# Kernel tuning notes

Measured on AMD Instinct MI355X. Metric: run time of the kernel, lower is better.

The kernel has to match this reference:

```python
import jax, jax.numpy as jnp
import numpy as np

NUM_EMBEDDINGS = 1024
EMBEDDING_DIM = 256
COMMITMENT_COST = 0.25


def setup_inputs() -> dict:
    key = jax.random.key(0)
    k1, k2 = jax.random.split(key)
    x = jax.random.normal(k1, (16, 4096, EMBEDDING_DIM), dtype=jnp.float32)
    # torch init: uniform(-1/K, 1/K); keep same scale
    embedding_weight = jax.random.uniform(
        k2, (NUM_EMBEDDINGS, EMBEDDING_DIM), dtype=jnp.float32,
        minval=-1.0 / NUM_EMBEDDINGS, maxval=1.0 / NUM_EMBEDDINGS)
    return {"x": x, "embedding_weight": embedding_weight}


def reference(x, embedding_weight):
    original_shape = x.shape
    x_flat = x.reshape(-1, EMBEDDING_DIM)                     # [N, D]
    d2 = (jnp.sum(x_flat ** 2, axis=1, keepdims=True)
          + jnp.sum(embedding_weight ** 2, axis=1)
          - 2.0 * x_flat @ embedding_weight.T)                # [N, K]
    d2 = jnp.maximum(d2, 0.0)
    encoding_indices = jnp.argmin(d2, axis=1)                 # [N]
    quantized_flat = embedding_weight[encoding_indices]        # [N, D]
    quantized = quantized_flat.reshape(original_shape)

    q_sg = jax.lax.stop_gradient(quantized)
    codebook_loss = jnp.mean((q_sg - x) ** 2)
    commitment_loss = jnp.mean((x - q_sg) ** 2)
    vq_total_loss = codebook_loss + COMMITMENT_COST * commitment_loss

    # straight-through estimator
    quantized_st = x + jax.lax.stop_gradient(quantized - x)

    # perplexity via index counts (avoids materializing one-hot [N, K])
    n = x_flat.shape[0]
    counts = jnp.zeros((NUM_EMBEDDINGS,), jnp.float32).at[encoding_indices].add(1.0)
    avg_probs = counts / n
    perplexity = jnp.exp(-jnp.sum(avg_probs * jnp.log(avg_probs + 1e-10)))

    return quantized_st, vq_total_loss, perplexity, encoding_indices
```

## Files before the change

### kernel.cpp

```cpp
#include <hip/hip_runtime.h>
#include <math.h>

#define N_ROWS   65536
#define DIM      256
#define KCODES   1024
#define Q_SIZE   (N_ROWS * DIM)
#define OUT_LOSS Q_SIZE
#define OUT_PERP (Q_SIZE + 1)
#define OUT_IDX  (Q_SIZE + 2)

#define TAUP 200.0f

#define WS_LOSS   0
#define WS_RCNT   8
#define WS_E2     16
#define WS_E2P    4112
#define WS_COUNTS 8208
#define WS_IDX    12304
#define WS_RLIST  274448
#define WS_ET     536592
#define WS_P      1585168

typedef _Float16 half8 __attribute__((ext_vector_type(8)));
typedef _Float16 half4 __attribute__((ext_vector_type(4)));
typedef float    f32x4 __attribute__((ext_vector_type(4)));

#define ROWB 528
#define RPB  64

#define LDS_X  0
#define LDS_E2 33792
#define LDS_B  37888

__global__ void k_prep(const float* __restrict__ E, float* __restrict__ e2,
                       float* __restrict__ e2p, float* __restrict__ Et,
                       _Float16* __restrict__ P,
                       int* __restrict__ counts, double* __restrict__ loss,
                       int* __restrict__ rcnt) {
    int b = blockIdx.x, t = threadIdx.x;
    __shared__ double red[256];
    float v = E[b * DIM + t];
    red[t] = (double)v * (double)v;

    {
        int o   = b * 256 + t;
        int j    = o & 7;
        int lane = (o >> 3) & 63;
        int nt   = (o >> 9) & 3;
        int kk   = (o >> 11) & 7;
        int cbq  = o >> 14;
        int q = cbq >> 2, cb = cbq & 3;
        int code = q * 256 + cb * 64 + nt * 16 + (lane & 15);
        int d    = (lane >> 4) * 8 + kk * 32 + j;
        P[o] = (_Float16)(E[code * DIM + d] * 1024.0f);
    }

    __syncthreads();
    for (int s = 128; s > 0; s >>= 1) {
        if (t < s) red[t] += red[t + s];
        __syncthreads();
    }
    if (t == 0) { e2[b] = (float)red[0]; e2p[b] = (float)(red[0] * 1048576.0); }

    int o = b * 256 + t;
    int d = o >> 10, k = o & 1023;
    Et[o] = E[k * DIM + d];

    if (b < 4) counts[b * 256 + t] = 0;
    if (b == 0 && t == 0) { *loss = 0.0; *rcnt = 0; }
}

__launch_bounds__(256)
__global__ void k_main(const float* __restrict__ X, const _Float16* __restrict__ P,
                       const float* __restrict__ e2p,
                       int* __restrict__ idx_ws, int* __restrict__ rlist,
                       int* __restrict__ rcnt) {
    __shared__ __align__(16) char sAll[70656];
    const int tid  = threadIdx.x;
    const int wid  = tid >> 6;
    const int lane = tid & 63;
    const int c16  = lane & 15;
    const int kg   = lane >> 4;
    const int rb   = blockIdx.x * RPB;

    char* sA = sAll + LDS_X;

    {
        const float4* Xg = (const float4*)(X + (size_t)rb * DIM);
        #pragma unroll
        for (int it = 0; it < 16; ++it) {
            int f = it * 256 + tid;
            int row = f >> 6, d4 = f & 63;
            float4 v = Xg[(size_t)row * 64 + d4];
            half4 hh = {(_Float16)v.x, (_Float16)v.y, (_Float16)v.z, (_Float16)v.w};
            *(half4*)(sA + row * ROWB + d4 * 8) = hh;
        }
        ((float4*)(sAll + LDS_E2))[tid] = ((const float4*)e2p)[tid];
    }

    const char* gB = (const char*)P + (size_t)wid * 131072 + (size_t)lane * 16;
    char*       lB = sAll + LDS_B + wid * 8192;
#define GLL(ss, nt)                                                                          \
    __builtin_amdgcn_global_load_lds(                                                        \
        (const __attribute__((address_space(1))) unsigned int*)(gB + (size_t)(((ss) * 4 + (nt)) * 1024)), \
        (__attribute__((address_space(3))) unsigned int*)(lB + (((ss) & 1) * 4096 + (nt) * 1024)),        \
        16, 0, 0)
    GLL(0, 0); GLL(0, 1); GLL(0, 2); GLL(0, 3);
    GLL(1, 0); GLL(1, 1); GLL(1, 2); GLL(1, 3);

    __syncthreads();

    int Abase[4];
    #pragma unroll
    for (int mt = 0; mt < 4; ++mt) Abase[mt] = (mt * 16 + c16) * ROWB + kg * 16;

    float tb1[16], tb2[16];
    int   ti1[16];
    #pragma unroll
    for (int i = 0; i < 16; ++i) { tb1[i] = 3.4e38f; tb2[i] = 3.4e38f; ti1[i] = 0; }

    const int cw = wid * 256;
    const float* sE2 = (const float*)(sAll + LDS_E2);

    f32x4 acc[4][4];

    #pragma unroll
    for (int s = 0; s < 32; ++s) {
        const int cb = s >> 3, kk = s & 7;
        if (kk == 0) {
            #pragma unroll
            for (int mt = 0; mt < 4; ++mt)
                #pragma unroll
                for (int nt = 0; nt < 4; ++nt) acc[mt][nt] = 0.0f;
        }
        if (s == 31) { asm volatile("s_waitcnt vmcnt(0)" ::: "memory"); }
        else         { asm volatile("s_waitcnt vmcnt(4)" ::: "memory"); }
        __builtin_amdgcn_sched_barrier(0);

        const char* bb = lB + (s & 1) * 4096 + (size_t)lane * 16;
        half8 b0 = *(const half8*)(bb);
        half8 b1 = *(const half8*)(bb + 1024);
        half8 b2 = *(const half8*)(bb + 2048);
        half8 b3 = *(const half8*)(bb + 3072);
        half8 ah[4];
        #pragma unroll
        for (int mt = 0; mt < 4; ++mt)
            ah[mt] = *(const half8*)(sA + Abase[mt] + kk * 64);

        asm volatile("s_waitcnt lgkmcnt(0)" ::: "memory");
        __builtin_amdgcn_sched_barrier(0);
        if (s < 30) { GLL(s + 2, 0); GLL(s + 2, 1); GLL(s + 2, 2); GLL(s + 2, 3); }
        __builtin_amdgcn_sched_barrier(0);

        #pragma unroll
        for (int mt = 0; mt < 4; ++mt) {
            acc[mt][0] = __builtin_amdgcn_mfma_f32_16x16x32_f16(ah[mt], b0, acc[mt][0], 0, 0, 0);
            acc[mt][1] = __builtin_amdgcn_mfma_f32_16x16x32_f16(ah[mt], b1, acc[mt][1], 0, 0, 0);
            acc[mt][2] = __builtin_amdgcn_mfma_f32_16x16x32_f16(ah[mt], b2, acc[mt][2], 0, 0, 0);
            acc[mt][3] = __builtin_amdgcn_mfma_f32_16x16x32_f16(ah[mt], b3, acc[mt][3], 0, 0, 0);
        }

        if (kk == 7) {
            const int cbase = cw + cb * 64;
            const int c0 = cbase + c16;
            float e2v[4];
            #pragma unroll
            for (int nt = 0; nt < 4; ++nt) e2v[nt] = sE2[c0 + nt * 16];
            #pragma unroll
            for (int mt = 0; mt < 4; ++mt)
                #pragma unroll
                for (int nt = 0; nt < 4; ++nt) {
                    int code = cbase + nt * 16 + c16;
                    #pragma unroll
                    for (int r = 0; r < 4; ++r) {
                        float sc = fmaf(-2048.0f, acc[mt][nt][r], e2v[nt]);
                        int ix = mt * 4 + r;
                        float hi = fmaxf(tb1[ix], sc);
                        tb2[ix] = fminf(tb2[ix], hi);
                        bool lt = sc < tb1[ix];
                        tb1[ix] = lt ? sc : tb1[ix];
                        ti1[ix] = lt ? code : ti1[ix];
                    }
                }
        }
    }
#undef GLL

    #pragma unroll
    for (int ix = 0; ix < 16; ++ix) {
        float v1 = tb1[ix], v2 = tb2[ix];
        int   j1 = ti1[ix];
        #pragma unroll
        for (int m = 1; m < 16; m <<= 1) {
            float ov1 = __shfl_xor(v1, m, 64);
            int   oj1 = __shfl_xor(j1, m, 64);
            float ov2 = __shfl_xor(v2, m, 64);
            bool take = (ov1 < v1) || (ov1 == v1 && oj1 < j1);
            float losr = take ? v1 : ov1;
            v1 = take ? ov1 : v1;
            j1 = take ? oj1 : j1;
            v2 = fminf(fminf(v2, ov2), losr);
        }
        tb1[ix] = v1; tb2[ix] = v2; ti1[ix] = j1;
    }

    __syncthreads();
    float* mB1 = (float*)sA;
    float* mB2 = (float*)(sA + 1024);
    int*   mI1 = (int*)(sA + 2048);
    #pragma unroll
    for (int ix = 0; ix < 16; ++ix) {
        if (c16 == ix) {
            int row = (ix >> 2) * 16 + kg * 4 + (ix & 3);
            mB1[row * 4 + wid] = tb1[ix];
            mB2[row * 4 + wid] = tb2[ix];
            mI1[row * 4 + wid] = ti1[ix];
        }
    }
    __syncthreads();
    if (tid < RPB) {
        float m1 = 3.4e38f, m2 = 3.4e38f;
        int mi = 0;
        #pragma unroll
        for (int w = 0; w < 4; ++w) {
            float v = mB1[tid * 4 + w];
            int  id = mI1[tid * 4 + w];
            float u = mB2[tid * 4 + w];
            bool take = (v < m1) || (v == m1 && id < mi);
            float losr = take ? m1 : v;
            m1 = take ? v : m1;
            mi = take ? id : mi;
            m2 = fminf(fminf(m2, u), losr);
        }
        int g = rb + tid;
        idx_ws[g] = mi;
        if (m2 - m1 < TAUP) {
            int slot = atomicAdd(rcnt, 1);
            rlist[slot] = g;
        }
    }
}

__launch_bounds__(256, 1)
__global__ void k_refine(const float* __restrict__ X, const float* __restrict__ Et,
                         const float* __restrict__ e2,
                         const int* __restrict__ rlist, const int* __restrict__ rcnt,
                         int* __restrict__ idx_ws) {
    __shared__ float xs[4][256];
    __shared__ float sbv[4][256];
    __shared__ int   sbi[4][256];
    __shared__ float x2s[4];
    __shared__ int   rows[4];
    const int cnt = *rcnt;
    const int t = threadIdx.x;
    for (int base = blockIdx.x * 4; base < cnt; base += gridDim.x * 4) {
        __syncthreads();
        if (t < 4) {
            int e = base + t;
            rows[t] = rlist[e < cnt ? e : (cnt - 1)];
        }
        __syncthreads();
        ((float4*)xs[t >> 6])[t & 63] =
            ((const float4*)(X + (size_t)rows[t >> 6] * DIM))[t & 63];
        __syncthreads();
        if (t < 4) {
            double s = 0.0;
            for (int d = 0; d < DIM; ++d) { double xv = (double)xs[t][d]; s += xv * xv; }
            x2s[t] = (float)s;
        }
        __syncthreads();

        double a0[4], a1[4], a2[4], a3[4];
        #pragma unroll
        for (int r = 0; r < 4; ++r) { a0[r] = 0.0; a1[r] = 0.0; a2[r] = 0.0; a3[r] = 0.0; }
        for (int d = 0; d < DIM; ++d) {
            double e0 = (double)Et[d * KCODES + t];
            double e1 = (double)Et[d * KCODES + 256 + t];
            double e2d = (double)Et[d * KCODES + 512 + t];
            double e3 = (double)Et[d * KCODES + 768 + t];
            #pragma unroll
            for (int r = 0; r < 4; ++r) {
                double xv = (double)xs[r][d];
                a0[r] += xv * e0;
                a1[r] += xv * e1;
                a2[r] += xv * e2d;
                a3[r] += xv * e3;
            }
        }

        const float eA = e2[t], eB = e2[256 + t], eC = e2[512 + t], eD = e2[768 + t];
        #pragma unroll
        for (int r = 0; r < 4; ++r) {
            float best = 3.4e38f; int bk = 0;
            float x2 = x2s[r];
            { float d2 = fmaf(-2.f, (float)a0[r], x2 + eA); if (d2 < best) { best = d2; bk = t; } }
            { float d2 = fmaf(-2.f, (float)a1[r], x2 + eB); if (d2 < best) { best = d2; bk = 256 + t; } }
            { float d2 = fmaf(-2.f, (float)a2[r], x2 + eC); if (d2 < best) { best = d2; bk = 512 + t; } }
            { float d2 = fmaf(-2.f, (float)a3[r], x2 + eD); if (d2 < best) { best = d2; bk = 768 + t; } }
            sbv[r][t] = best; sbi[r][t] = bk;
        }
        __syncthreads();
        {
            const int w = t >> 6, lane = t & 63;
            float v = sbv[w][lane];     int id = sbi[w][lane];
            #pragma unroll
            for (int c = 1; c < 4; ++c) {
                float ov = sbv[w][lane + 64 * c]; int oi = sbi[w][lane + 64 * c];
                if (ov < v || (ov == v && oi < id)) { v = ov; id = oi; }
            }
            #pragma unroll
            for (int m = 1; m < 64; m <<= 1) {
                float ov = __shfl_xor(v, m, 64);
                int   oi = __shfl_xor(id, m, 64);
                if (ov < v || (ov == v && oi < id)) { v = ov; id = oi; }
            }
            if (lane == 0 && base + w < cnt) idx_ws[rows[w]] = id;
        }
    }
}

__launch_bounds__(256)
__global__ void k_out(const float* __restrict__ X, const float* __restrict__ E,
                      const int* __restrict__ idx_ws, float* __restrict__ out,
                      int* __restrict__ counts, double* __restrict__ loss) {
    const int tid = threadIdx.x;
    const int w = tid >> 6, lane = tid & 63;
    const int rbase = blockIdx.x * 64;
    double ls = 0.0;
    #pragma unroll 4
    for (int it = 0; it < 16; ++it) {
        const int row = rbase + it * 4 + w;
        const int k = idx_ws[row];
        float4 q = ((const float4*)(E + (size_t)k * DIM))[lane];
        float4 x = ((const float4*)(X + (size_t)row * DIM))[lane];
        ((float4*)(out + (size_t)row * DIM))[lane] = q;
        double d0 = (double)q.x - (double)x.x;
        double d1 = (double)q.y - (double)x.y;
        double d2 = (double)q.z - (double)x.z;
        double d3 = (double)q.w - (double)x.w;
        ls += d0 * d0 + d1 * d1 + d2 * d2 + d3 * d3;
        if (lane == 0) {
            atomicAdd(&counts[k], 1);
            out[OUT_IDX + row] = (float)k;
        }
    }
    __shared__ double red[256];
    red[tid] = ls;
    __syncthreads();
    for (int s = 128; s > 0; s >>= 1) {
        if (tid < s) red[tid] += red[tid + s];
        __syncthreads();
    }
    if (tid == 0) atomicAdd(loss, red[0]);
}

__global__ void k_fin(const int* __restrict__ counts, const double* __restrict__ loss,
                      float* __restrict__ out) {
    int t = threadIdx.x;
    __shared__ double red[256];
    double h = 0.0;
    #pragma unroll
    for (int i = 0; i < 4; ++i) {
        double p = (double)counts[t + i * 256] / (double)N_ROWS;
        h += p * log(p + 1e-10);
    }
    red[t] = h;
    __syncthreads();
    for (int s = 128; s > 0; s >>= 1) {
        if (t < s) red[t] += red[t + s];
        __syncthreads();
    }
    if (t == 0) {
        out[OUT_PERP] = (float)exp(-red[0]);
        out[OUT_LOSS] = (float)((*loss) / (double)Q_SIZE * 1.25);
    }
}

extern "C" void kernel_launch(void* const* d_in, const int* in_sizes, int n_in,
                              void* d_out, int out_size, void* d_ws, size_t ws_size,
                              hipStream_t stream) {
    (void)in_sizes; (void)n_in; (void)out_size; (void)ws_size;
    const float* X = (const float*)d_in[0];
    const float* E = (const float*)d_in[1];
    float* out = (float*)d_out;
    char* ws = (char*)d_ws;

    double*    loss   = (double*)(ws + WS_LOSS);
    int*       rcnt   = (int*)(ws + WS_RCNT);
    float*     e2     = (float*)(ws + WS_E2);
    float*     e2p    = (float*)(ws + WS_E2P);
    int*       counts = (int*)(ws + WS_COUNTS);
    int*       idx_ws = (int*)(ws + WS_IDX);
    int*       rlist  = (int*)(ws + WS_RLIST);
    float*     Et     = (float*)(ws + WS_ET);
    _Float16*  Pp     = (_Float16*)(ws + WS_P);

    k_prep<<<1024, 256, 0, stream>>>(E, e2, e2p, Et, Pp, counts, loss, rcnt);
    k_main<<<N_ROWS / RPB, 256, 0, stream>>>(X, Pp, e2p, idx_ws, rlist, rcnt);
    k_refine<<<512, 256, 0, stream>>>(X, Et, e2, rlist, rcnt, idx_ws);
    k_out<<<1024, 256, 0, stream>>>(X, E, idx_ws, out, counts, loss);
    k_fin<<<1, 256, 0, stream>>>(counts, loss, out);
}
```

Before: 198.4 us.

## Load codebook fragments directly into registers instead of staging through LDS

```diff
diff --git a/kernel.cpp b/kernel.cpp
--- a/kernel.cpp
+++ b/kernel.cpp
@@ -30,7 +30,6 @@
 
 #define LDS_X  0
 #define LDS_E2 33792
-#define LDS_B  37888
 
 __global__ void k_prep(const float* __restrict__ E, float* __restrict__ e2,
                        float* __restrict__ e2p, float* __restrict__ Et,
@@ -75,7 +74,7 @@
                        const float* __restrict__ e2p,
                        int* __restrict__ idx_ws, int* __restrict__ rlist,
                        int* __restrict__ rcnt) {
-    __shared__ __align__(16) char sAll[70656];
+    __shared__ __align__(16) char sAll[37888];
     const int tid  = threadIdx.x;
     const int wid  = tid >> 6;
     const int lane = tid & 63;
@@ -97,18 +96,18 @@
         }
         ((float4*)(sAll + LDS_E2))[tid] = ((const float4*)e2p)[tid];
     }
+    __syncthreads();
 
     const char* gB = (const char*)P + (size_t)wid * 131072 + (size_t)lane * 16;
-    char*       lB = sAll + LDS_B + wid * 8192;
-#define GLL(ss, nt)                                                                          \
-    __builtin_amdgcn_global_load_lds(                                                        \
-        (const __attribute__((address_space(1))) unsigned int*)(gB + (size_t)(((ss) * 4 + (nt)) * 1024)), \
-        (__attribute__((address_space(3))) unsigned int*)(lB + (((ss) & 1) * 4096 + (nt) * 1024)),        \
-        16, 0, 0)
-    GLL(0, 0); GLL(0, 1); GLL(0, 2); GLL(0, 3);
-    GLL(1, 0); GLL(1, 1); GLL(1, 2); GLL(1, 3);
-
-    __syncthreads();
+#define GLOAD(dst, ss, nt)                                                    \
+    asm volatile("global_load_dwordx4 %0, %1, off"                            \
+                 : "=v"(dst)                                                  \
+                 : "v"(gB + (size_t)(((ss) * 4 + (nt)) * 1024))               \
+                 : "memory")
+
+    half8 bA[4], bB[4], bC[4];
+    GLOAD(bA[0], 0, 0); GLOAD(bA[1], 0, 1); GLOAD(bA[2], 0, 2); GLOAD(bA[3], 0, 3);
+    GLOAD(bB[0], 1, 0); GLOAD(bB[1], 1, 1); GLOAD(bB[2], 1, 2); GLOAD(bB[3], 1, 3);
 
     int Abase[4];
     #pragma unroll
@@ -137,27 +136,22 @@
         else         { asm volatile("s_waitcnt vmcnt(4)" ::: "memory"); }
         __builtin_amdgcn_sched_barrier(0);
 
-        const char* bb = lB + (s & 1) * 4096 + (size_t)lane * 16;
-        half8 b0 = *(const half8*)(bb);
-        half8 b1 = *(const half8*)(bb + 1024);
-        half8 b2 = *(const half8*)(bb + 2048);
-        half8 b3 = *(const half8*)(bb + 3072);
+        if (s < 30) {
+            GLOAD(bC[0], s + 2, 0); GLOAD(bC[1], s + 2, 1);
+            GLOAD(bC[2], s + 2, 2); GLOAD(bC[3], s + 2, 3);
+        }
+
         half8 ah[4];
         #pragma unroll
         for (int mt = 0; mt < 4; ++mt)
             ah[mt] = *(const half8*)(sA + Abase[mt] + kk * 64);
 
-        asm volatile("s_waitcnt lgkmcnt(0)" ::: "memory");
-        __builtin_amdgcn_sched_barrier(0);
-        if (s < 30) { GLL(s + 2, 0); GLL(s + 2, 1); GLL(s + 2, 2); GLL(s + 2, 3); }
-        __builtin_amdgcn_sched_barrier(0);
-
         #pragma unroll
         for (int mt = 0; mt < 4; ++mt) {
-            acc[mt][0] = __builtin_amdgcn_mfma_f32_16x16x32_f16(ah[mt], b0, acc[mt][0], 0, 0, 0);
-            acc[mt][1] = __builtin_amdgcn_mfma_f32_16x16x32_f16(ah[mt], b1, acc[mt][1], 0, 0, 0);
-            acc[mt][2] = __builtin_amdgcn_mfma_f32_16x16x32_f16(ah[mt], b2, acc[mt][2], 0, 0, 0);
-            acc[mt][3] = __builtin_amdgcn_mfma_f32_16x16x32_f16(ah[mt], b3, acc[mt][3], 0, 0, 0);
+            acc[mt][0] = __builtin_amdgcn_mfma_f32_16x16x32_f16(ah[mt], bA[0], acc[mt][0], 0, 0, 0);
+            acc[mt][1] = __builtin_amdgcn_mfma_f32_16x16x32_f16(ah[mt], bA[1], acc[mt][1], 0, 0, 0);
+            acc[mt][2] = __builtin_amdgcn_mfma_f32_16x16x32_f16(ah[mt], bA[2], acc[mt][2], 0, 0, 0);
+            acc[mt][3] = __builtin_amdgcn_mfma_f32_16x16x32_f16(ah[mt], bA[3], acc[mt][3], 0, 0, 0);
         }
 
         if (kk == 7) {
@@ -175,16 +169,18 @@
                     for (int r = 0; r < 4; ++r) {
                         float sc = fmaf(-2048.0f, acc[mt][nt][r], e2v[nt]);
                         int ix = mt * 4 + r;
-                        float hi = fmaxf(tb1[ix], sc);
-                        tb2[ix] = fminf(tb2[ix], hi);
+                        tb2[ix] = __builtin_amdgcn_fmed3f(tb1[ix], tb2[ix], sc);
                         bool lt = sc < tb1[ix];
                         tb1[ix] = lt ? sc : tb1[ix];
                         ti1[ix] = lt ? code : ti1[ix];
                     }
                 }
         }
-    }
-#undef GLL
+
+        #pragma unroll
+        for (int nt = 0; nt < 4; ++nt) { bA[nt] = bB[nt]; bB[nt] = bC[nt]; }
+    }
+#undef GLOAD
 
     #pragma unroll
     for (int ix = 0; ix < 16; ++ix) {
@@ -273,6 +269,7 @@
         double a0[4], a1[4], a2[4], a3[4];
         #pragma unroll
         for (int r = 0; r < 4; ++r) { a0[r] = 0.0; a1[r] = 0.0; a2[r] = 0.0; a3[r] = 0.0; }
+        #pragma unroll 4
         for (int d = 0; d < DIM; ++d) {
             double e0 = (double)Et[d * KCODES + t];
             double e1 = (double)Et[d * KCODES + 256 + t];
@@ -397,7 +394,7 @@
 
     k_prep<<<1024, 256, 0, stream>>>(E, e2, e2p, Et, Pp, counts, loss, rcnt);
     k_main<<<N_ROWS / RPB, 256, 0, stream>>>(X, Pp, e2p, idx_ws, rlist, rcnt);
-    k_refine<<<512, 256, 0, stream>>>(X, Et, e2, rlist, rcnt, idx_ws);
+    k_refine<<<1024, 256, 0, stream>>>(X, Et, e2, rlist, rcnt, idx_ws);
     k_out<<<1024, 256, 0, stream>>>(X, E, idx_ws, out, counts, loss);
     k_fin<<<1, 256, 0, stream>>>(counts, loss, out);
 }
```

Result: faster. 169.1 us (-14.8%).
